# Performance work log

Hardware: AMD Instinct MI355X
Metric: run time of the kernel (lower is better)

## Reference

```python
import jax, jax.numpy as jnp
import numpy as np

B, T, D = 2, 4096, 1024      # batch, seq, hidden_dim
E, I = 16, 512               # n_routed_experts, expert_intermediate
K = 2                        # n_activated_experts
IS = 2048                    # shared_expert_intermediate
ALPHA = 1e-4                 # balance_loss_alpha
EPS = 1e-9


def setup_inputs() -> dict:
    key = jax.random.key(0)
    ks = jax.random.split(key, 8)
    s = lambda k, shape, fan: jax.random.normal(k, shape, jnp.float32) * (fan ** -0.5)
    return {
        "x": jax.random.normal(ks[0], (B, T, D), jnp.float32),
        "gate_w": s(ks[1], (D, E), D),            # router gate (no bias)
        "expert_bias": jnp.zeros((E,), jnp.float32),
        "sh_gate": s(ks[2], (D, IS), D),          # shared expert SwiGLU
        "sh_up": s(ks[3], (D, IS), D),
        "sh_down": s(ks[4], (IS, D), IS),
        "ex_gate": s(ks[5], (E, D, I), D),        # routed experts (stacked)
        "ex_up": s(ks[6], (E, D, I), D),
        "ex_down": s(ks[7], (E, I, D), I),
    }


def _swiglu(x, wg, wu, wd):
    return (jax.nn.silu(x @ wg) * (x @ wu)) @ wd


def reference(x, gate_w, expert_bias, sh_gate, sh_up, sh_down, ex_gate, ex_up, ex_down):
    Bq, Tq, Dq = x.shape
    # shared expert path (n_shared_experts = 1)
    shared = _swiglu(x, sh_gate, sh_up, sh_down)

    xf = x.reshape(Bq * Tq, Dq)                       # (N, D)
    N = xf.shape[0]

    # --- router: sigmoid gating, bias-adjusted top-k, normalized gates ---
    affinity = jax.nn.sigmoid(xf @ gate_w)            # (N, E)
    scores = affinity + expert_bias[None, :]
    _, idx = jax.lax.top_k(scores, K)                 # (N, K) int
    gv = jnp.take_along_axis(affinity, idx, axis=1)   # (N, K) gathered from affinity
    gv = gv / (gv.sum(-1, keepdims=True) + EPS)

    # --- balance loss (sequence-wise, Eq. 17-20) ---
    expert_mask = jax.nn.one_hot(idx, E, dtype=jnp.float32).sum(1)  # (N, E)
    f = expert_mask.sum(0) * E / (K * N)
    P = (affinity / (affinity.sum(-1, keepdims=True) + EPS)).mean(0)
    balance_loss = ALPHA * (f * P).sum()
    expert_counts = expert_mask.sum(0).astype(jnp.int32)            # (E,)

    # --- dispatch/compute/combine, expressed as dense combine-weight matrix ---
    # w[n, e] = sum of gate values for token n routed to expert e (same math
    # as the masked gather/scatter loop in the original)
    w = jnp.zeros((N, E), jnp.float32).at[jnp.arange(N)[:, None], idx].add(gv)
    h = jax.nn.silu(jnp.einsum('nd,edi->eni', xf, ex_gate)) \
        * jnp.einsum('nd,edi->eni', xf, ex_up)        # (E, N, I)
    routed = jnp.einsum('ne,eni,eid->nd', w, h, ex_down)  # (N, D)
    routed = routed.reshape(Bq, Tq, Dq)

    output = shared + routed  # note: original does NOT add residual despite docstring
    return output, balance_loss, expert_counts
```

## Files before the change

kernel.cpp:

```cpp
#include <hip/hip_runtime.h>
#include <stdint.h>

#define NTOK 8192
#define DDIM 1024
#define NEXP 16
#define KSEL 2
#define ISH 2048
#define IEX 512
#define ALPHAC 1e-4f
#define REPS 1e-9f

typedef __attribute__((ext_vector_type(8))) short short8;
typedef __attribute__((ext_vector_type(4))) float f32x4;

__device__ __forceinline__ unsigned short f2bf(float f){
  union { float f; uint32_t u; } v; v.f = f;
  uint32_t u = v.u;
  uint32_t r = (u + 0x7fffu + ((u >> 16) & 1u)) >> 16;
  return (unsigned short)r;
}
__device__ __forceinline__ float bf2f(unsigned short h){
  union { uint32_t u; float f; } v; v.u = ((uint32_t)h) << 16; return v.f;
}

__device__ __forceinline__ void gload16(const void* g, void* l){
  __builtin_amdgcn_global_load_lds(
      (const __attribute__((address_space(1))) void*)g,
      (__attribute__((address_space(3))) void*)l, 16, 0, 0);
}

__global__ __launch_bounds__(256) void convert_f32_bf16(const float* __restrict__ in,
                                                        unsigned short* __restrict__ out){
  int id = blockIdx.x * 256 + threadIdx.x;
  float4 v = ((const float4*)in)[id];
  ushort4 o;
  o.x = f2bf(v.x); o.y = f2bf(v.y); o.z = f2bf(v.z); o.w = f2bf(v.w);
  ((ushort4*)out)[id] = o;
}

template<int RM, int RO>
__global__ __launch_bounds__(256) void transpose_bf16(const float* __restrict__ in,
                                                      unsigned short* __restrict__ outp,
                                                      int R, int C){
  __shared__ float tile[64][65];
  const float* ip = in + (size_t)blockIdx.z * R * C;
  unsigned short* op = outp + (size_t)blockIdx.z * R * C * RM;
  int c0 = blockIdx.x * 64, r0 = blockIdx.y * 64;
  int t = threadIdx.x;
  int tr = t >> 4, tc = (t & 15) * 4;
  #pragma unroll
  for (int i = 0; i < 4; ++i){
    float4 v = *(const float4*)&ip[(size_t)(r0 + tr + i*16) * C + c0 + tc];
    tile[tr + i*16][tc+0] = v.x;
    tile[tr + i*16][tc+1] = v.y;
    tile[tr + i*16][tc+2] = v.z;
    tile[tr + i*16][tc+3] = v.w;
  }
  __syncthreads();
  #pragma unroll
  for (int i = 0; i < 4; ++i){
    int oc = tr + i*16;
    ushort4 w;
    w.x = f2bf(tile[tc+0][oc]);
    w.y = f2bf(tile[tc+1][oc]);
    w.z = f2bf(tile[tc+2][oc]);
    w.w = f2bf(tile[tc+3][oc]);
    *(ushort4*)&op[(size_t)((c0 + oc) * RM + RO) * R + r0 + tc] = w;
  }
}

__global__ __launch_bounds__(256) void logits_kernel(
    const float* __restrict__ x, const float* __restrict__ gw,
    float* __restrict__ logits)
{
  __shared__ float gws[16][1024];
  const int t = threadIdx.x;
  #pragma unroll
  for (int k = 0; k < 16; ++k){
    int idx = t + k * 256;
    float4 v = ((const float4*)gw)[idx];
    int d = idx >> 2, e0 = (idx & 3) * 4;
    gws[e0+0][d] = v.x;
    gws[e0+1][d] = v.y;
    gws[e0+2][d] = v.z;
    gws[e0+3][d] = v.w;
  }
  __syncthreads();
  const int lane = t & 63, w = t >> 6;
  const int nb = blockIdx.x * 16 + w * 4;
  for (int i = 0; i < 4; ++i){
    const int n = nb + i;
    const float4* xr = (const float4*)(x + (size_t)n * DDIM);
    float4 xv[4];
    #pragma unroll
    for (int k = 0; k < 4; ++k) xv[k] = xr[lane + k*64];
    float acc[16];
    #pragma unroll
    for (int e = 0; e < 16; ++e){
      float s = 0.f;
      #pragma unroll
      for (int k = 0; k < 4; ++k){
        float4 g = *(const float4*)&gws[e][(lane + k*64)*4];
        s = fmaf(xv[k].x, g.x, fmaf(xv[k].y, g.y, fmaf(xv[k].z, g.z, fmaf(xv[k].w, g.w, s))));
      }
      acc[e] = s;
    }
    #pragma unroll
    for (int m = 1; m < 64; m <<= 1)
      #pragma unroll
      for (int e = 0; e < 16; ++e)
        acc[e] += __shfl_xor(acc[e], m);
    if (lane == 0){
      float4* op = (float4*)(logits + (size_t)n * 16);
      op[0] = make_float4(acc[0],  acc[1],  acc[2],  acc[3]);
      op[1] = make_float4(acc[4],  acc[5],  acc[6],  acc[7]);
      op[2] = make_float4(acc[8],  acc[9],  acc[10], acc[11]);
      op[3] = make_float4(acc[12], acc[13], acc[14], acc[15]);
    }
  }
}

__global__ __launch_bounds__(256) void router_finish(
    const float* __restrict__ logits, const float* __restrict__ ebias,
    int* __restrict__ idxb, float* __restrict__ gvb,
    float* __restrict__ Ppart, int* __restrict__ Cpart)
{
  __shared__ float Ps[16];
  __shared__ int Cs[16];
  const int t = threadIdx.x;
  if (t < 16){ Ps[t] = 0.f; Cs[t] = 0; }
  __syncthreads();
  const int lane = t & 63;
  const int n = blockIdx.x * 256 + t;
  const float4* lp = (const float4*)(logits + (size_t)n * 16);
  float4 a0 = lp[0], a1 = lp[1], a2 = lp[2], a3 = lp[3];
  float aff[16];
  aff[0]=a0.x; aff[1]=a0.y; aff[2]=a0.z; aff[3]=a0.w;
  aff[4]=a1.x; aff[5]=a1.y; aff[6]=a1.z; aff[7]=a1.w;
  aff[8]=a2.x; aff[9]=a2.y; aff[10]=a2.z; aff[11]=a2.w;
  aff[12]=a3.x; aff[13]=a3.y; aff[14]=a3.z; aff[15]=a3.w;
  float rowsum = REPS;
  #pragma unroll
  for (int e = 0; e < 16; ++e){
    aff[e] = 1.f / (1.f + __expf(-aff[e]));
    rowsum += aff[e];
  }
  float bj[16];
  #pragma unroll
  for (int e = 0; e < 16; ++e) bj[e] = ebias[e];
  float bestS = aff[0] + bj[0], bestA = aff[0]; int i1 = 0;
  #pragma unroll
  for (int j = 1; j < 16; ++j){
    float sc = aff[j] + bj[j];
    bool gt2 = sc > bestS;
    bestS = gt2 ? sc : bestS; bestA = gt2 ? aff[j] : bestA; i1 = gt2 ? j : i1;
  }
  float secS = -1e30f, secA = 0.f; int i2 = 0;
  #pragma unroll
  for (int j = 0; j < 16; ++j){
    float sc = aff[j] + bj[j];
    bool ok = (j != i1) && (sc > secS);
    secS = ok ? sc : secS; secA = ok ? aff[j] : secA; i2 = ok ? j : i2;
  }
  float den = bestA + secA + REPS;
  idxb[n*2]   = i1; idxb[n*2+1] = i2;
  gvb[n*2]    = bestA / den; gvb[n*2+1] = secA / den;

  float inv = 1.f / rowsum;
  float pv[16]; int cv[16];
  #pragma unroll
  for (int e = 0; e < 16; ++e){
    pv[e] = aff[e] * inv;
    cv[e] = (e == i1) + (e == i2);
  }
  #pragma unroll
  for (int m = 1; m < 64; m <<= 1)
    #pragma unroll
    for (int e = 0; e < 16; ++e){
      pv[e] += __shfl_xor(pv[e], m);
      cv[e] += __shfl_xor(cv[e], m);
    }
  if (lane == 0){
    #pragma unroll
    for (int e = 0; e < 16; ++e){
      atomicAdd(&Ps[e], pv[e]);
      atomicAdd(&Cs[e], cv[e]);
    }
  }
  __syncthreads();
  if (t < 16){ Ppart[blockIdx.x*16 + t] = Ps[t]; Cpart[blockIdx.x*16 + t] = Cs[t]; }
}

__global__ __launch_bounds__(256) void finalize2(
    const float* __restrict__ Ppart, const int* __restrict__ Cpart,
    int* __restrict__ counts, int* __restrict__ offs, int* __restrict__ cursor,
    float* __restrict__ out_tail)
{
  __shared__ float P[16];
  __shared__ int C[16];
  int t = threadIdx.x;
  if (t < 16){ P[t] = 0.f; C[t] = 0; }
  __syncthreads();
  if (t < 32){
    int e = t & 15, c = t >> 4;
    float p = 0.f; int cc = 0;
    for (int b = c * 16; b < c * 16 + 16; ++b){ p += Ppart[b*16 + e]; cc += Cpart[b*16 + e]; }
    atomicAdd(&P[e], p); atomicAdd(&C[e], cc);
  }
  __syncthreads();
  if (t == 0){
    int a = 0; float loss = 0.f;
    for (int i = 0; i < 16; ++i){
      offs[i] = a; cursor[i] = a; counts[i] = C[i]; a += C[i];
      loss += ((float)C[i] * (float)NEXP / (float)(KSEL * NTOK)) * (P[i] / (float)NTOK);
      out_tail[1+i] = (float)C[i];
    }
    out_tail[0] = ALPHAC * loss;
  }
}

__global__ __launch_bounds__(256) void slot_assign(
    const int* __restrict__ idxb, const float* __restrict__ gvb,
    int* __restrict__ cursor, int* __restrict__ tokp, float* __restrict__ gatep,
    int* __restrict__ rslot)
{
  int i = blockIdx.x * 256 + threadIdx.x;
  int e = idxb[i];
  int s = atomicAdd(&cursor[e], 1);
  tokp[s] = i >> 1;
  gatep[s] = gvb[i];
  rslot[i] = s;
}

template<bool GROUPED, bool GATHER, int MODE, int NYT>
__global__ __launch_bounds__(256, 2) void gemm128(
    const unsigned short* __restrict__ A,
    const unsigned short* __restrict__ B,
    const unsigned short* __restrict__ comp,
    void* __restrict__ Cout,
    int M, int N, int K,
    const int* __restrict__ counts,
    const int* __restrict__ offsets,
    const int* __restrict__ perm,
    const float* __restrict__ rowscale)
{
  __shared__ __align__(16) unsigned short As[2][128*64];
  __shared__ __align__(16) unsigned short Bs[2][128*64];

  const int nwg = gridDim.x;
  const int bid = blockIdx.x;
  const int wg = (bid & 7) * (nwg >> 3) + (bid >> 3);
  const int mtl = wg / NYT;
  const int nt  = wg % NYT;

  int mt = mtl, off = 0, cnt = M;
  const unsigned short* bp = B;
  if (GROUPED){
    int acc = 0, e = -1;
    #pragma unroll
    for (int i = 0; i < NEXP; ++i){
      int c = counts[i]; int tt = (c + 127) >> 7;
      if (e < 0 && mtl < acc + tt){ e = i; mt = mtl - acc; off = offsets[i]; cnt = c; }
      acc += tt;
    }
    if (e < 0) return;
    bp += (size_t)e * N * K;
  }
  const int m0 = mt * 128, n0 = nt * 128;
  const int t = threadIdx.x;
  const int lane = t & 63;
  const int wid = t >> 6;
  const int wm = (wid >> 1) * 64;
  const int wn = (wid & 1) * 64;
  const int l15 = lane & 15, g = lane >> 4;

  const unsigned short* asrc[4];
  const unsigned short* bsrc[4];
  int ldso[4];
  #pragma unroll
  for (int c = 0; c < 4; ++c){
    int s = (wid*4 + c)*64 + lane;
    int row = s >> 3, c16 = s & 7;
    int scol = (c16 ^ (row & 7)) * 8;
    ldso[c] = (wid*4 + c) * 512;
    int r = m0 + row;
    int rc = GROUPED ? (r < cnt ? r : (cnt > 0 ? cnt - 1 : 0)) : r;
    int ar;
    if (GATHER) ar = perm[off + rc];
    else        ar = GROUPED ? off + rc : rc;
    asrc[c] = A + (size_t)ar * K + scol;
    bsrc[c] = bp + (size_t)(n0 + row) * K + scol;
  }

  f32x4 acc[4][4];
  #pragma unroll
  for (int i = 0; i < 4; ++i)
    #pragma unroll
    for (int j = 0; j < 4; ++j)
      #pragma unroll
      for (int r = 0; r < 4; ++r) acc[i][j][r] = 0.f;

  auto STAGE = [&](int buf, int k0){
    #pragma unroll
    for (int c = 0; c < 4; ++c) gload16(asrc[c] + k0, (void*)&As[buf][ldso[c]]);
    #pragma unroll
    for (int c = 0; c < 4; ++c) gload16(bsrc[c] + k0, (void*)&Bs[buf][ldso[c]]);
  };

  const int ntk = K >> 6;
  STAGE(0, 0);
  __syncthreads();
  int cur = 0;
  for (int tk = 0; tk < ntk; ++tk){
    if (tk + 1 < ntk) STAGE(cur ^ 1, (tk + 1) << 6);
    #pragma unroll
    for (int ks = 0; ks < 2; ++ks){
      short8 af[4], bf[4];
      #pragma unroll
      for (int i = 0; i < 4; ++i){
        int row = wm + i * 16 + l15;
        af[i] = *(const short8*)&As[cur][row * 64 + (((ks*4 + g) ^ (row & 7)) * 8)];
      }
      #pragma unroll
      for (int j = 0; j < 4; ++j){
        int row = wn + j * 16 + l15;
        bf[j] = *(const short8*)&Bs[cur][row * 64 + (((ks*4 + g) ^ (row & 7)) * 8)];
      }
      #pragma unroll
      for (int i = 0; i < 4; ++i)
        #pragma unroll
        for (int j = 0; j < 4; ++j)
          acc[i][j] = __builtin_amdgcn_mfma_f32_16x16x32_bf16(af[i], bf[j], acc[i][j], 0, 0, 0);
    }
    __syncthreads();
    cur ^= 1;
  }

  #pragma unroll
  for (int i = 0; i < 4; ++i)
    #pragma unroll
    for (int j = 0; j < 4; ++j)
      #pragma unroll
      for (int r = 0; r < 4; ++r){
        int lr = wm + i * 16 + g * 4 + r;
        int grow = m0 + lr;
        if (GROUPED && grow >= cnt) continue;
        int gcol = n0 + wn + j * 16 + l15;
        size_t orow = GROUPED ? (size_t)(off + grow) : (size_t)grow;
        float val = acc[i][j][r];
        if (MODE == 1){
          ((float*)Cout)[orow * N + gcol] = val;
        } else if (MODE == 6){
          float uo = __shfl_xor(val, 1);
          if (!(l15 & 1)){
            float rv = val / (1.f + __expf(-val)) * uo;
            ((unsigned short*)Cout)[orow * (N >> 1) + (gcol >> 1)] = f2bf(rv);
          }
        } else {
          if (MODE == 2) val *= rowscale[off + grow];
          if (MODE == 4) val = val / (1.f + __expf(-val));
          if (MODE == 5) val *= bf2f(comp[orow * N + gcol]);
          ((unsigned short*)Cout)[orow * N + gcol] = f2bf(val);
        }
      }
}

__global__ __launch_bounds__(256) void combine_kernel(float* __restrict__ out,
                                                      const unsigned short* __restrict__ ybuf,
                                                      const int* __restrict__ rs){
  int id = blockIdx.x * 256 + threadIdx.x;
  int n = id >> 8;
  int q = id & 255;
  int s0 = rs[n*2], s1 = rs[n*2+1];
  float4 o = ((float4*)out)[id];
  ushort4 a = ((const ushort4*)(ybuf + (size_t)s0 * DDIM))[q];
  ushort4 b = ((const ushort4*)(ybuf + (size_t)s1 * DDIM))[q];
  o.x += bf2f(a.x) + bf2f(b.x);
  o.y += bf2f(a.y) + bf2f(b.y);
  o.z += bf2f(a.z) + bf2f(b.z);
  o.w += bf2f(a.w) + bf2f(b.w);
  ((float4*)out)[id] = o;
}

extern "C" void kernel_launch(void* const* d_in, const int* in_sizes, int n_in,
                              void* d_out, int out_size, void* d_ws, size_t ws_size,
                              hipStream_t stream)
{
  const float* x       = (const float*)d_in[0];
  const float* gate_w  = (const float*)d_in[1];
  const float* ebias   = (const float*)d_in[2];
  const float* sh_gate = (const float*)d_in[3];
  const float* sh_up   = (const float*)d_in[4];
  const float* sh_down = (const float*)d_in[5];
  const float* ex_gate = (const float*)d_in[6];
  const float* ex_up   = (const float*)d_in[7];
  const float* ex_down = (const float*)d_in[8];
  float* out = (float*)d_out;
  (void)in_sizes; (void)n_in; (void)out_size; (void)ws_size;

  size_t o = 0;
  auto alloc = [&](size_t bytes) -> void* {
    o = (o + 255) & ~(size_t)255;
    void* p = (char*)d_ws + o;
    o += bytes;
    return p;
  };
  unsigned short* xb    = (unsigned short*)alloc((size_t)NTOK*DDIM*2);
  unsigned short* shgT  = (unsigned short*)alloc((size_t)ISH*DDIM*2);
  unsigned short* shuT  = (unsigned short*)alloc((size_t)ISH*DDIM*2);
  unsigned short* shdT  = (unsigned short*)alloc((size_t)DDIM*ISH*2);
  unsigned short* exguT = (unsigned short*)alloc((size_t)NEXP*2*IEX*DDIM*2);
  unsigned short* exdT  = (unsigned short*)alloc((size_t)NEXP*DDIM*IEX*2);
  unsigned short* hbuf  = (unsigned short*)alloc((size_t)NTOK*KSEL*IEX*2);
  unsigned short* big   = (unsigned short*)alloc((size_t)NTOK*ISH*2);
  float* logits = (float*)alloc((size_t)NTOK*NEXP*4);
  int*   idxb  = (int*)alloc(NTOK*KSEL*4);
  float* gvb   = (float*)alloc(NTOK*KSEL*4);
  float* Ppart = (float*)alloc(32*16*4);
  int*   Cpart = (int*)alloc(32*16*4);
  int*   counts= (int*)alloc(64);
  int*   offs  = (int*)alloc(64);
  int*   cursor= (int*)alloc(64);
  int*   tokp  = (int*)alloc(NTOK*KSEL*4);
  float* gatep = (float*)alloc(NTOK*KSEL*4);
  int*   rslot = (int*)alloc(NTOK*KSEL*4);

  convert_f32_bf16<<<NTOK*DDIM/1024, 256, 0, stream>>>(x, xb);
  transpose_bf16<1,0><<<dim3(ISH/64,  DDIM/64, 1),    256, 0, stream>>>(sh_gate, shgT, DDIM, ISH);
  transpose_bf16<1,0><<<dim3(ISH/64,  DDIM/64, 1),    256, 0, stream>>>(sh_up,   shuT, DDIM, ISH);
  transpose_bf16<1,0><<<dim3(DDIM/64, ISH/64,  1),    256, 0, stream>>>(sh_down, shdT, ISH, DDIM);
  transpose_bf16<2,0><<<dim3(IEX/64,  DDIM/64, NEXP), 256, 0, stream>>>(ex_gate, exguT, DDIM, IEX);
  transpose_bf16<2,1><<<dim3(IEX/64,  DDIM/64, NEXP), 256, 0, stream>>>(ex_up,   exguT, DDIM, IEX);
  transpose_bf16<1,0><<<dim3(DDIM/64, IEX/64,  NEXP), 256, 0, stream>>>(ex_down, exdT, IEX, DDIM);

  logits_kernel<<<512, 256, 0, stream>>>(x, gate_w, logits);
  router_finish<<<32, 256, 0, stream>>>(logits, ebias, idxb, gvb, Ppart, Cpart);
  finalize2<<<1, 256, 0, stream>>>(Ppart, Cpart, counts, offs, cursor,
                                   out + (size_t)NTOK*DDIM);
  slot_assign<<<NTOK*KSEL/256, 256, 0, stream>>>(idxb, gvb, cursor, tokp, gatep, rslot);

  gemm128<false,false,4,16><<<64*16, 256, 0, stream>>>(
      xb, shgT, nullptr, big, NTOK, ISH, DDIM, nullptr, nullptr, nullptr, nullptr);
  gemm128<false,false,5,16><<<64*16, 256, 0, stream>>>(
      xb, shuT, big, big, NTOK, ISH, DDIM, nullptr, nullptr, nullptr, nullptr);
  gemm128<false,false,1,8><<<64*8, 256, 0, stream>>>(
      big, shdT, nullptr, out, NTOK, DDIM, ISH, nullptr, nullptr, nullptr, nullptr);

  gemm128<true,true,6,8><<<144*8, 256, 0, stream>>>(
      xb, exguT, nullptr, hbuf, 0, 2*IEX, DDIM, counts, offs, tokp, nullptr);
  gemm128<true,false,2,8><<<144*8, 256, 0, stream>>>(
      hbuf, exdT, nullptr, big, 0, DDIM, IEX, counts, offs, nullptr, gatep);

  combine_kernel<<<NTOK*DDIM/1024, 256, 0, stream>>>(out, big, rslot);
}
```

Baseline: 413.0 us.

## Enlarge GEMM tiles to 256x256 and fuse shared gate/up GEMMs

Replaces the 128x128 GEMM kernel with a 256x256 tile kernel using 512 threads (8 waves, each computing 128x64), which raises arithmetic intensity per LDS byte. The shared-expert gate and up weights are interleaved into one matrix so a single GEMM produces the SwiGLU activation directly, removing one launch and the intermediate round trip through the big buffer. The trade-offs are 128KB of LDS per block with one block per CU, more register pressure, and fewer blocks, which could hurt load balance, especially for the grouped expert GEMMs with larger padding per expert.

Measured after the change: 457.3 us. +10.7%, slower.

```diff
diff --git a/kernel.cpp b/kernel.cpp
--- a/kernel.cpp
+++ b/kernel.cpp
@@ -233,10 +233,9 @@
 }
 
 template<bool GROUPED, bool GATHER, int MODE, int NYT>
-__global__ __launch_bounds__(256, 2) void gemm128(
+__global__ __launch_bounds__(512, 1) void gemm256(
     const unsigned short* __restrict__ A,
     const unsigned short* __restrict__ B,
-    const unsigned short* __restrict__ comp,
     void* __restrict__ Cout,
     int M, int N, int K,
     const int* __restrict__ counts,
@@ -244,45 +243,45 @@
     const int* __restrict__ perm,
     const float* __restrict__ rowscale)
 {
-  __shared__ __align__(16) unsigned short As[2][128*64];
-  __shared__ __align__(16) unsigned short Bs[2][128*64];
+  __shared__ __align__(16) unsigned short As[2][256*64];
+  __shared__ __align__(16) unsigned short Bs[2][256*64];
 
   const int nwg = gridDim.x;
   const int bid = blockIdx.x;
   const int wg = (bid & 7) * (nwg >> 3) + (bid >> 3);
   const int mtl = wg / NYT;
-  const int nt  = wg % NYT;
+  const int ntc = wg % NYT;
 
   int mt = mtl, off = 0, cnt = M;
   const unsigned short* bp = B;
   if (GROUPED){
-    int acc = 0, e = -1;
+    int acc_ = 0, e = -1;
     #pragma unroll
     for (int i = 0; i < NEXP; ++i){
-      int c = counts[i]; int tt = (c + 127) >> 7;
-      if (e < 0 && mtl < acc + tt){ e = i; mt = mtl - acc; off = offsets[i]; cnt = c; }
-      acc += tt;
+      int c = counts[i]; int tt = (c + 255) >> 8;
+      if (e < 0 && mtl < acc_ + tt){ e = i; mt = mtl - acc_; off = offsets[i]; cnt = c; }
+      acc_ += tt;
     }
     if (e < 0) return;
     bp += (size_t)e * N * K;
   }
-  const int m0 = mt * 128, n0 = nt * 128;
+  const int m0 = mt * 256, n0 = ntc * 256;
   const int t = threadIdx.x;
   const int lane = t & 63;
   const int wid = t >> 6;
-  const int wm = (wid >> 1) * 64;
-  const int wn = (wid & 1) * 64;
+  const int wm0 = (wid >> 2) * 128;
+  const int wn0 = (wid & 3) * 64;
   const int l15 = lane & 15, g = lane >> 4;
 
   const unsigned short* asrc[4];
   const unsigned short* bsrc[4];
-  int ldso[4];
+  int ldst[4];
   #pragma unroll
   for (int c = 0; c < 4; ++c){
-    int s = (wid*4 + c)*64 + lane;
-    int row = s >> 3, c16 = s & 7;
+    int slot = c * 512 + t;
+    int row = slot >> 3, c16 = slot & 7;
     int scol = (c16 ^ (row & 7)) * 8;
-    ldso[c] = (wid*4 + c) * 512;
+    ldst[c] = slot * 8;
     int r = m0 + row;
     int rc = GROUPED ? (r < cnt ? r : (cnt > 0 ? cnt - 1 : 0)) : r;
     int ar;
@@ -292,19 +291,20 @@
     bsrc[c] = bp + (size_t)(n0 + row) * K + scol;
   }
 
-  f32x4 acc[4][4];
-  #pragma unroll
-  for (int i = 0; i < 4; ++i)
+  f32x4 acc[8][4];
+  #pragma unroll
+  for (int i = 0; i < 8; ++i)
     #pragma unroll
     for (int j = 0; j < 4; ++j)
       #pragma unroll
       for (int r = 0; r < 4; ++r) acc[i][j][r] = 0.f;
 
-  auto STAGE = [&](int buf, int k0){
-    #pragma unroll
-    for (int c = 0; c < 4; ++c) gload16(asrc[c] + k0, (void*)&As[buf][ldso[c]]);
-    #pragma unroll
-    for (int c = 0; c < 4; ++c) gload16(bsrc[c] + k0, (void*)&Bs[buf][ldso[c]]);
+  auto STAGE = [&](int buf, int kt){
+    const int k0 = kt << 6;
+    #pragma unroll
+    for (int c = 0; c < 4; ++c) gload16(asrc[c] + k0, (void*)&As[buf][ldst[c]]);
+    #pragma unroll
+    for (int c = 0; c < 4; ++c) gload16(bsrc[c] + k0, (void*)&Bs[buf][ldst[c]]);
   };
 
   const int ntk = K >> 6;
@@ -312,42 +312,43 @@
   __syncthreads();
   int cur = 0;
   for (int tk = 0; tk < ntk; ++tk){
-    if (tk + 1 < ntk) STAGE(cur ^ 1, (tk + 1) << 6);
-    #pragma unroll
-    for (int ks = 0; ks < 2; ++ks){
-      short8 af[4], bf[4];
-      #pragma unroll
-      for (int i = 0; i < 4; ++i){
-        int row = wm + i * 16 + l15;
-        af[i] = *(const short8*)&As[cur][row * 64 + (((ks*4 + g) ^ (row & 7)) * 8)];
+    if (tk + 1 < ntk) STAGE(cur ^ 1, tk + 1);
+    short8 bfr[4][2];
+    #pragma unroll
+    for (int j = 0; j < 4; ++j)
+      #pragma unroll
+      for (int ks = 0; ks < 2; ++ks){
+        int row = wn0 + j * 16 + l15;
+        bfr[j][ks] = *(const short8*)&Bs[cur][row * 64 + (((ks*4 + g) ^ (row & 7)) * 8)];
       }
-      #pragma unroll
-      for (int j = 0; j < 4; ++j){
-        int row = wn + j * 16 + l15;
-        bf[j] = *(const short8*)&Bs[cur][row * 64 + (((ks*4 + g) ^ (row & 7)) * 8)];
-      }
-      #pragma unroll
-      for (int i = 0; i < 4; ++i)
-        #pragma unroll
-        for (int j = 0; j < 4; ++j)
-          acc[i][j] = __builtin_amdgcn_mfma_f32_16x16x32_bf16(af[i], bf[j], acc[i][j], 0, 0, 0);
+    #pragma unroll
+    for (int mi = 0; mi < 8; ++mi){
+      int row = wm0 + mi * 16 + l15;
+      short8 af0 = *(const short8*)&As[cur][row * 64 + (((0 + g) ^ (row & 7)) * 8)];
+      short8 af1 = *(const short8*)&As[cur][row * 64 + (((4 + g) ^ (row & 7)) * 8)];
+      #pragma unroll
+      for (int j = 0; j < 4; ++j)
+        acc[mi][j] = __builtin_amdgcn_mfma_f32_16x16x32_bf16(af0, bfr[j][0], acc[mi][j], 0, 0, 0);
+      #pragma unroll
+      for (int j = 0; j < 4; ++j)
+        acc[mi][j] = __builtin_amdgcn_mfma_f32_16x16x32_bf16(af1, bfr[j][1], acc[mi][j], 0, 0, 0);
     }
     __syncthreads();
     cur ^= 1;
   }
 
   #pragma unroll
-  for (int i = 0; i < 4; ++i)
+  for (int mi = 0; mi < 8; ++mi)
     #pragma unroll
     for (int j = 0; j < 4; ++j)
       #pragma unroll
       for (int r = 0; r < 4; ++r){
-        int lr = wm + i * 16 + g * 4 + r;
+        int lr = wm0 + mi * 16 + g * 4 + r;
         int grow = m0 + lr;
         if (GROUPED && grow >= cnt) continue;
-        int gcol = n0 + wn + j * 16 + l15;
+        int gcol = n0 + wn0 + j * 16 + l15;
         size_t orow = GROUPED ? (size_t)(off + grow) : (size_t)grow;
-        float val = acc[i][j][r];
+        float val = acc[mi][j][r];
         if (MODE == 1){
           ((float*)Cout)[orow * N + gcol] = val;
         } else if (MODE == 6){
@@ -357,9 +358,7 @@
             ((unsigned short*)Cout)[orow * (N >> 1) + (gcol >> 1)] = f2bf(rv);
           }
         } else {
-          if (MODE == 2) val *= rowscale[off + grow];
-          if (MODE == 4) val = val / (1.f + __expf(-val));
-          if (MODE == 5) val *= bf2f(comp[orow * N + gcol]);
+          val *= rowscale[off + grow];
           ((unsigned short*)Cout)[orow * N + gcol] = f2bf(val);
         }
       }
@@ -406,8 +405,7 @@
     return p;
   };
   unsigned short* xb    = (unsigned short*)alloc((size_t)NTOK*DDIM*2);
-  unsigned short* shgT  = (unsigned short*)alloc((size_t)ISH*DDIM*2);
-  unsigned short* shuT  = (unsigned short*)alloc((size_t)ISH*DDIM*2);
+  unsigned short* shguT = (unsigned short*)alloc((size_t)2*ISH*DDIM*2);
   unsigned short* shdT  = (unsigned short*)alloc((size_t)DDIM*ISH*2);
   unsigned short* exguT = (unsigned short*)alloc((size_t)NEXP*2*IEX*DDIM*2);
   unsigned short* exdT  = (unsigned short*)alloc((size_t)NEXP*DDIM*IEX*2);
@@ -426,8 +424,8 @@
   int*   rslot = (int*)alloc(NTOK*KSEL*4);
 
   convert_f32_bf16<<<NTOK*DDIM/1024, 256, 0, stream>>>(x, xb);
-  transpose_bf16<1,0><<<dim3(ISH/64,  DDIM/64, 1),    256, 0, stream>>>(sh_gate, shgT, DDIM, ISH);
-  transpose_bf16<1,0><<<dim3(ISH/64,  DDIM/64, 1),    256, 0, stream>>>(sh_up,   shuT, DDIM, ISH);
+  transpose_bf16<2,0><<<dim3(ISH/64,  DDIM/64, 1),    256, 0, stream>>>(sh_gate, shguT, DDIM, ISH);
+  transpose_bf16<2,1><<<dim3(ISH/64,  DDIM/64, 1),    256, 0, stream>>>(sh_up,   shguT, DDIM, ISH);
   transpose_bf16<1,0><<<dim3(DDIM/64, ISH/64,  1),    256, 0, stream>>>(sh_down, shdT, ISH, DDIM);
   transpose_bf16<2,0><<<dim3(IEX/64,  DDIM/64, NEXP), 256, 0, stream>>>(ex_gate, exguT, DDIM, IEX);
   transpose_bf16<2,1><<<dim3(IEX/64,  DDIM/64, NEXP), 256, 0, stream>>>(ex_up,   exguT, DDIM, IEX);
@@ -439,17 +437,15 @@
                                    out + (size_t)NTOK*DDIM);
   slot_assign<<<NTOK*KSEL/256, 256, 0, stream>>>(idxb, gvb, cursor, tokp, gatep, rslot);
 
-  gemm128<false,false,4,16><<<64*16, 256, 0, stream>>>(
-      xb, shgT, nullptr, big, NTOK, ISH, DDIM, nullptr, nullptr, nullptr, nullptr);
-  gemm128<false,false,5,16><<<64*16, 256, 0, stream>>>(
-      xb, shuT, big, big, NTOK, ISH, DDIM, nullptr, nullptr, nullptr, nullptr);
-  gemm128<false,false,1,8><<<64*8, 256, 0, stream>>>(
-      big, shdT, nullptr, out, NTOK, DDIM, ISH, nullptr, nullptr, nullptr, nullptr);
-
-  gemm128<true,true,6,8><<<144*8, 256, 0, stream>>>(
-      xb, exguT, nullptr, hbuf, 0, 2*IEX, DDIM, counts, offs, tokp, nullptr);
-  gemm128<true,false,2,8><<<144*8, 256, 0, stream>>>(
-      hbuf, exdT, nullptr, big, 0, DDIM, IEX, counts, offs, nullptr, gatep);
+  gemm256<false,false,6,16><<<32*16, 512, 0, stream>>>(
+      xb, shguT, big, NTOK, 2*ISH, DDIM, nullptr, nullptr, nullptr, nullptr);
+  gemm256<false,false,1,4><<<32*4, 512, 0, stream>>>(
+      big, shdT, out, NTOK, DDIM, ISH, nullptr, nullptr, nullptr, nullptr);
+
+  gemm256<true,true,6,4><<<80*4, 512, 0, stream>>>(
+      xb, exguT, hbuf, 0, 2*IEX, DDIM, counts, offs, tokp, nullptr);
+  gemm256<true,false,2,4><<<80*4, 512, 0, stream>>>(
+      hbuf, exdT, big, 0, DDIM, IEX, counts, offs, nullptr, gatep);
 
   combine_kernel<<<NTOK*DDIM/1024, 256, 0, stream>>>(out, big, rslot);
 }
```
